# Kernel tuning notes

Measured on AMD Instinct MI355X. Metric: run time of the kernel, lower is better.

The kernel has to match this reference:

```python
import jax, jax.numpy as jnp
import numpy as np

N, C, T, V, S = 64, 64, 300, 25, 3
INTER = C // 4  # coff_embedding = 4
KER_T = 9      # temporal attention kernel
KER_V = V      # V=25 is odd -> spatial attention kernel = V, pad = (V-1)//2


def setup_inputs() -> dict:
    key = jax.random.key(0)
    ks = jax.random.split(key, 20)
    f = lambda k, s, scale=0.05: jax.random.normal(k, s, jnp.float32) * scale
    return {
        "x": jax.random.normal(ks[0], (N, C, T, V), jnp.float32),
        "A": f(ks[1], (S, V, V), 0.2),
        "alpha": jnp.array(0.1, jnp.float32),
        "Wa": f(ks[2], (S, INTER, C)), "ba": f(ks[3], (S, INTER)),
        "Wb": f(ks[4], (S, INTER, C)), "bb": f(ks[5], (S, INTER)),
        "Wd": f(ks[6], (S, C, C)),     "bd": f(ks[7], (S, C)),
        "bn_gamma": jnp.ones((C,), jnp.float32),
        "bn_beta": jnp.zeros((C,), jnp.float32),
        "bn_mean": f(ks[8], (C,)),
        "bn_var": jax.random.uniform(ks[9], (C,), jnp.float32) + 0.5,
        "Wsa": f(ks[10], (1, C, KER_V)), "bsa": f(ks[11], (1,)),
        "Wta": f(ks[12], (1, C, KER_T)), "bta": f(ks[13], (1,)),
        "Wfc1": f(ks[14], (C // 2, C)),  "bfc1": f(ks[15], (C // 2,)),
        "Wfc2": f(ks[16], (C, C // 2)),  "bfc2": f(ks[17], (C,)),
    }


def _conv1d(z, w, bias, pad):
    # z: [N, Cin, L], w: [Cout, Cin, K] -> [N, Cout, L]
    o = jax.lax.conv_general_dilated(z, w, (1,), [(pad, pad)],
                                     dimension_numbers=('NCH', 'OIH', 'NCH'))
    return o + bias[None, :, None]


def reference(x, A, alpha, Wa, ba, Wb, bb, Wd, bd,
              bn_gamma, bn_beta, bn_mean, bn_var,
              Wsa, bsa, Wta, bta, Wfc1, bfc1, Wfc2, bfc2):
    n, c, t, v = x.shape
    inter = Wa.shape[1]
    # adaptive adjacency per subset (1x1 convs = channel einsums)
    a = jnp.einsum('nctv,sic->nsitv', x, Wa) + ba[None, :, :, None, None]   # [N,S,inter,T,V]
    b = jnp.einsum('nctv,sic->nsitv', x, Wb) + bb[None, :, :, None, None]
    M = jnp.tanh(jnp.einsum('nsitv,nsitw->nsvw', a, b) / (inter * t))       # [N,S,V,V]
    G = A[None] + alpha * M
    # graph conv: x @ G per subset, then 1x1 conv_d, summed over subsets
    zp = jnp.einsum('nctv,nsvw->nsctw', x, G)                                # [N,S,C,T,V]
    y = jnp.einsum('nsctv,soc->notv', zp, Wd) + bd.sum(0)[None, :, None, None]
    # BN (eval) + residual (down = identity since in_c == out_c) + ReLU
    inv = bn_gamma / jnp.sqrt(bn_var + 1e-5)
    y = (y - bn_mean[None, :, None, None]) * inv[None, :, None, None] + bn_beta[None, :, None, None]
    y = jax.nn.relu(y + x)
    # spatial attention over joints
    se1 = jax.nn.sigmoid(_conv1d(y.mean(2), Wsa, bsa, (KER_V - 1) // 2))    # [N,1,V]
    y = y * se1[:, :, None, :] + y
    # temporal attention over frames
    se1 = jax.nn.sigmoid(_conv1d(y.mean(3), Wta, bta, (KER_T - 1) // 2))    # [N,1,T]
    y = y * se1[:, :, :, None] + y
    # channel attention (squeeze-excite)
    se = y.mean((2, 3))                                                      # [N,C]
    se2 = jax.nn.sigmoid(jax.nn.relu(se @ Wfc1.T + bfc1) @ Wfc2.T + bfc2)
    y = y * se2[:, :, None, None] + y
    return y
```

## Files before the change

kernel.cpp:

```cpp
#include <hip/hip_runtime.h>

typedef __bf16 bf16;
typedef bf16 bf16x8 __attribute__((ext_vector_type(8)));
typedef bf16 bf16x4 __attribute__((ext_vector_type(4)));
typedef float f32x4 __attribute__((ext_vector_type(4)));

#define WS_XG    0u
#define WS_WAB   61505536u
#define WS_WD    61517824u
#define WS_COEFA 61542400u
#define WS_COEFB 61542656u
#define WS_GT    61542912u
#define WS_MPART 61936128u
#define WS_STP   61936128u
#define WS_SVP   68489728u
#define WS_SE1   74519040u
#define WS_SE2   74527232u
#define WS_SE3   74605056u

__device__ __forceinline__ f32x4 mfma16(bf16x8 a, bf16x8 b, f32x4 c) {
  return __builtin_amdgcn_mfma_f32_16x16x32_bf16(a, b, c, 0, 0, 0);
}

__global__ __launch_bounds__(256) void k_prep(
    const float* __restrict__ Wa, const float* __restrict__ Wb,
    const float* __restrict__ Wd, const float* __restrict__ bd,
    const float* __restrict__ gam, const float* __restrict__ bet,
    const float* __restrict__ mean, const float* __restrict__ var,
    char* __restrict__ ws) {
  bf16* wab = (bf16*)(ws + WS_WAB);
  bf16* wd  = (bf16*)(ws + WS_WD);
  float* cA = (float*)(ws + WS_COEFA);
  float* cB = (float*)(ws + WS_COEFB);
  int tid = threadIdx.x;
  for (int f = tid; f < 3*32*64; f += 256) {
    int s = f >> 11, r = (f >> 6) & 31, c = f & 63;
    float v = (r < 16) ? Wa[(s*16 + r)*64 + c] : Wb[(s*16 + (r-16))*64 + c];
    wab[f] = (bf16)v;
  }
  for (int f = tid; f < 3*64*64; f += 256) wd[f] = (bf16)Wd[f];
  if (tid < 64) {
    float bds = bd[tid] + bd[64+tid] + bd[128+tid];
    float iv = gam[tid] / sqrtf(var[tid] + 1e-5f);
    cA[tid] = iv;
    cB[tid] = (bds - mean[tid]) * iv + bet[tid];
  }
}

__global__ __launch_bounds__(256) void k_tr(
    const float* __restrict__ x, char* __restrict__ ws) {
  __shared__ __attribute__((aligned(16))) bf16 tile[64*204];
  const int tc = blockIdx.x, n = blockIdx.y, tid = threadIdx.x;
  const int t0 = tc*8;
  const int vmax = min(200, 7500 - t0*25);
  bf16* XG = (bf16*)(ws + WS_XG);
  #pragma unroll
  for (int it = 0; it < 13; ++it) {
    int u = it*256 + tid;
    if (u < 3200) {
      int c = u / 50, q = u % 50;
      int idx = 4*q;
      if (idx < vmax) {
        float4 val = *(const float4*)(x + (size_t)(n*64 + c)*7500 + t0*25 + idx);
        bf16x4 pk = {(bf16)val.x, (bf16)val.y, (bf16)val.z, (bf16)val.w};
        *(bf16x4*)&tile[c*204 + idx] = pk;
      }
    }
  }
  __syncthreads();
  #pragma unroll
  for (int it = 0; it < 7; ++it) {
    int u = it*256 + tid;
    if (u < 1600) {
      int c8 = u & 7, tv = u >> 3;
      int t = t0 + tv/25, v = tv % 25;
      if (t < 300) {
        bf16x8 pk;
        #pragma unroll
        for (int j = 0; j < 8; ++j) pk[j] = tile[(c8*8 + j)*204 + tv];
        *(bf16x8*)&XG[((size_t)(n*300 + t)*25 + v)*64 + c8*8] = pk;
      }
    }
  }
}

__global__ __launch_bounds__(256) void k1_m(
    const float* __restrict__ ba_g, const float* __restrict__ bb_g,
    char* __restrict__ ws) {
  __shared__ __attribute__((aligned(16))) bf16 AB[6*32*72];
  const int seg = blockIdx.x, n = blockIdx.y;
  const int tid = threadIdx.x;
  const int lane = tid & 63, wv = tid >> 6;
  const int l15 = lane & 15, l4 = lane >> 4;
  const int t0 = seg*19, tlen = min(19, 300 - t0);
  const bf16* XG  = (const bf16*)(ws + WS_XG);
  const bf16* wab = (const bf16*)(ws + WS_WAB);
  const f32x4 z4 = {0.f,0.f,0.f,0.f};

  bf16x8 Afr[6][2];
  float bias[6][4];
  #pragma unroll
  for (int rt = 0; rt < 6; ++rt) {
    const int s = rt >> 1, abk = rt & 1;
    #pragma unroll
    for (int kk = 0; kk < 2; ++kk)
      Afr[rt][kk] = *(const bf16x8*)&wab[(s*32 + abk*16 + l15)*64 + kk*32 + 8*l4];
    const float* bp = abk ? bb_g : ba_g;
    #pragma unroll
    for (int r = 0; r < 4; ++r) bias[rt][r] = bp[s*16 + 4*l4 + r];
  }
  f32x4 macc[3]; macc[0]=z4; macc[1]=z4; macc[2]=z4;
  const int vt2 = wv >> 1, wt2 = wv & 1;
  const int nch = (tlen + 3) >> 2;

  for (int ch = 0; ch < nch; ++ch) {
    const int tl = ch*4 + wv;
    const int t = t0 + tl;
    const bool tv = (tl < tlen);
    #pragma unroll
    for (int vt = 0; vt < 2; ++vt) {
      f32x4 acc[6];
      #pragma unroll
      for (int rt = 0; rt < 6; ++rt) acc[rt] = z4;
      #pragma unroll
      for (int kk = 0; kk < 2; ++kk) {
        bf16x8 B = *(const bf16x8*)&XG[((size_t)(n*300 + t)*25 + vt*16 + l15)*64 + kk*32 + 8*l4];
        #pragma unroll
        for (int rt = 0; rt < 6; ++rt) acc[rt] = mfma16(Afr[rt][kk], B, acc[rt]);
      }
      #pragma unroll
      for (int rt = 0; rt < 6; ++rt) {
        bf16x4 pk;
        #pragma unroll
        for (int r = 0; r < 4; ++r)
          pk[r] = (bf16)(tv ? (acc[rt][r] + bias[rt][r]) : 0.f);
        *(bf16x4*)&AB[(rt*32 + vt*16 + l15)*72 + wv*16 + 4*l4] = pk;
      }
    }
    __syncthreads();
    #pragma unroll
    for (int s = 0; s < 3; ++s) {
      #pragma unroll
      for (int kk = 0; kk < 2; ++kk) {
        bf16x8 Aa = *(const bf16x8*)&AB[((s*2 + 0)*32 + vt2*16 + l15)*72 + kk*32 + 8*l4];
        bf16x8 Bb = *(const bf16x8*)&AB[((s*2 + 1)*32 + wt2*16 + l15)*72 + kk*32 + 8*l4];
        macc[s] = mfma16(Aa, Bb, macc[s]);
      }
    }
    __syncthreads();
  }
  float* mp = (float*)(ws + WS_MPART);
  #pragma unroll
  for (int s = 0; s < 3; ++s) {
    #pragma unroll
    for (int r = 0; r < 4; ++r) {
      int v = vt2*16 + 4*l4 + r, w = wt2*16 + l15;
      mp[(((n*16 + seg)*3 + s)*32 + v)*32 + w] = macc[s][r];
    }
  }
}

__global__ __launch_bounds__(256) void k1b_g(
    const float* __restrict__ A, const float* __restrict__ alp,
    char* __restrict__ ws) {
  int e = blockIdx.x*256 + threadIdx.x;
  int w = e & 31, v = (e >> 5) & 31;
  int s = (e >> 10) % 3, n = e / 3072;
  const float* mp = (const float*)(ws + WS_MPART);
  float m = 0.f;
  #pragma unroll
  for (int p = 0; p < 16; ++p)
    m += mp[(((n*16 + p)*3 + s)*32 + v)*32 + w];
  float g = 0.f;
  if (v < 25 && w < 25)
    g = A[(s*25 + v)*25 + w] + alp[0] * tanhf(m * (1.f/4800.f));
  bf16* gt = (bf16*)(ws + WS_GT);
  gt[((n*3 + s)*32 + w)*32 + v] = (bf16)g;
}

__global__ __launch_bounds__(256, 4) void k3_y(char* __restrict__ ws) {
  __shared__ __attribute__((aligned(16))) bf16 wdL[3*64*72];
  __shared__ __attribute__((aligned(16))) bf16 ULs[4*16*96];
  const int seg = blockIdx.x, n = blockIdx.y;
  const int tid = threadIdx.x, lane = tid & 63, wv = tid >> 6;
  const int l15 = lane & 15, l4 = lane >> 4;
  const int t0 = seg*19, tlen = min(19, 300 - t0);
  const bf16* XG = (const bf16*)(ws + WS_XG);
  bf16* YG = (bf16*)(ws + WS_XG);
  const bf16* wd = (const bf16*)(ws + WS_WD);
  const bf16* gt = (const bf16*)(ws + WS_GT);
  const float* cA = (const float*)(ws + WS_COEFA);
  const float* cB = (const float*)(ws + WS_COEFB);
  const f32x4 z4 = {0.f,0.f,0.f,0.f};
  bf16* UL = &ULs[wv*16*96];

  for (int f = tid; f < 1536; f += 256) {
    int row = f >> 3, c8 = f & 7;
    *(bf16x8*)&wdL[row*72 + c8*8] = *(const bf16x8*)&wd[row*64 + c8*8];
  }
  bf16x8 Gfr[2][3];
  #pragma unroll
  for (int wt = 0; wt < 2; ++wt)
    #pragma unroll
    for (int s = 0; s < 3; ++s)
      Gfr[wt][s] = *(const bf16x8*)&gt[((n*3 + s)*32 + wt*16 + l15)*32 + 8*l4];
  __syncthreads();

  const int tb = (tlen*wv) >> 2, te = (tlen*(wv+1)) >> 2;
  float st[4][2][4] = {};

  for (int tl = tb; tl < te; ++tl) {
    const size_t rowb = (size_t)(n*300 + t0 + tl)*25;
    bf16x8 Bv[2][2];
    #pragma unroll
    for (int vt = 0; vt < 2; ++vt)
      #pragma unroll
      for (int kk = 0; kk < 2; ++kk)
        Bv[vt][kk] = *(const bf16x8*)&XG[(rowb + vt*16 + l15)*64 + kk*32 + 8*l4];
    #pragma unroll
    for (int ot = 0; ot < 4; ++ot) {
      #pragma unroll
      for (int s = 0; s < 3; ++s) {
        bf16x8 W0 = *(const bf16x8*)&wdL[(s*64 + ot*16 + l15)*72 + 8*l4];
        bf16x8 W1 = *(const bf16x8*)&wdL[(s*64 + ot*16 + l15)*72 + 32 + 8*l4];
        #pragma unroll
        for (int vt = 0; vt < 2; ++vt) {
          f32x4 acc = mfma16(W0, Bv[vt][0], z4);
          acc = mfma16(W1, Bv[vt][1], acc);
          #pragma unroll
          for (int r = 0; r < 4; ++r)
            UL[(4*l4 + r)*96 + s*32 + vt*16 + l15] = (bf16)acc[r];
        }
      }
      f32x4 acc2[2] = {z4, z4};
      #pragma unroll
      for (int s = 0; s < 3; ++s) {
        bf16x8 Aa = *(const bf16x8*)&UL[l15*96 + s*32 + 8*l4];
        acc2[0] = mfma16(Aa, Gfr[0][s], acc2[0]);
        acc2[1] = mfma16(Aa, Gfr[1][s], acc2[1]);
      }
      const int o0 = ot*16 + 4*l4;
      const f32x4 cAr = *(const f32x4*)&cA[o0];
      const f32x4 cBr = *(const f32x4*)&cB[o0];
      #pragma unroll
      for (int wt = 0; wt < 2; ++wt) {
        const int w = wt*16 + l15;
        bf16x4 Rx = *(const bf16x4*)&XG[(rowb + w)*64 + o0];
        if (w < 25) {
          bf16x4 pk;
          #pragma unroll
          for (int r = 0; r < 4; ++r) {
            float val = fmaxf(acc2[wt][r]*cAr[r] + cBr[r] + (float)Rx[r], 0.f);
            pk[r] = (bf16)val;
            st[ot][wt][r] += val;
          }
          *(bf16x4*)&YG[(rowb + w)*64 + o0] = pk;
        }
      }
    }
  }
  float* LDSf = (float*)wdL;
  float* stp = (float*)(ws + WS_STP);
  #pragma unroll
  for (int half = 0; half < 2; ++half) {
    __syncthreads();
    #pragma unroll
    for (int ot2 = 0; ot2 < 2; ++ot2)
      #pragma unroll
      for (int wt = 0; wt < 2; ++wt)
        #pragma unroll
        for (int r = 0; r < 4; ++r)
          LDSf[wv*1056 + (ot2*16 + 4*l4 + r)*33 + wt*16 + l15] = st[half*2 + ot2][wt][r];
    __syncthreads();
    for (int e = tid; e < 800; e += 256) {
      int o = e / 25, w = e % 25;
      float sum = LDSf[o*33 + w] + LDSf[1056 + o*33 + w]
                + LDSf[2112 + o*33 + w] + LDSf[3168 + o*33 + w];
      stp[((n*16 + seg)*64 + half*32 + o)*25 + w] = sum;
    }
  }
}

__global__ __launch_bounds__(256) void k4_se1(
    const float* __restrict__ Wsa, const float* __restrict__ bsa,
    char* __restrict__ ws) {
  __shared__ float Sm[64][26];
  __shared__ float red[25][8];
  int n = blockIdx.x, tid = threadIdx.x;
  const float* stp = (const float*)(ws + WS_STP);
  for (int f = tid; f < 1600; f += 256) {
    int c = f / 25, v = f % 25;
    float s = 0.f;
    #pragma unroll
    for (int p = 0; p < 16; ++p) s += stp[((n*16 + p)*64 + c)*25 + v];
    Sm[c][v] = s * (1.f/300.f);
  }
  __syncthreads();
  float acc = 0.f;
  int v = tid >> 3, part = tid & 7;
  if (tid < 200) {
    for (int c = part; c < 64; c += 8) {
      #pragma unroll
      for (int k = 0; k < 25; ++k) {
        int vv = v + k - 12;
        if (vv >= 0 && vv < 25) acc += Wsa[c*25 + k] * Sm[c][vv];
      }
    }
    red[v][part] = acc;
  }
  __syncthreads();
  if (tid < 25) {
    float a = bsa[0];
    #pragma unroll
    for (int p = 0; p < 8; ++p) a += red[tid][p];
    ((float*)(ws + WS_SE1))[n*32 + tid] = 1.f + 1.f/(1.f + expf(-a));
  }
}

__global__ __launch_bounds__(256) void k5_sv(char* __restrict__ ws) {
  __shared__ float w1[25];
  const int tq = blockIdx.x, n = blockIdx.y;
  const int wv = threadIdx.x >> 6, lane = threadIdx.x & 63;
  const bf16* YG = (const bf16*)(ws + WS_XG);
  bf16* svp = (bf16*)(ws + WS_SVP);
  if (threadIdx.x < 25) w1[threadIdx.x] = ((const float*)(ws + WS_SE1))[n*32 + threadIdx.x];
  __syncthreads();
  const int tb = tq*75;
  for (int i = wv; i < 75; i += 4) {
    const int t = tb + i;
    float acc = 0.f;
    #pragma unroll
    for (int v = 0; v < 25; ++v)
      acc += w1[v] * (float)YG[(((size_t)n*300 + t)*25 + v)*64 + lane];
    svp[((size_t)n*304 + t)*64 + lane] = (bf16)acc;
  }
}

__global__ __launch_bounds__(1024) void k_att2(
    const float* __restrict__ Wta, const float* __restrict__ bta,
    const float* __restrict__ Wfc1, const float* __restrict__ bfc1,
    const float* __restrict__ Wfc2, const float* __restrict__ bfc2,
    char* __restrict__ ws) {
  __shared__ bf16 Sv[64][304];
  __shared__ float WLa[576];
  __shared__ float redt[304][4];
  __shared__ float w2s[304];
  __shared__ float red2[64][16];
  __shared__ float mS[64];
  __shared__ float hS[32];
  const int n = blockIdx.x, tid = threadIdx.x;
  const bf16* svp = (const bf16*)(ws + WS_SVP);

  for (int u = tid; u < 300*64; u += 1024) {
    int t = u >> 6, c = u & 63;
    Sv[c][t] = svp[((size_t)n*304 + t)*64 + c];
  }
  for (int f = tid; f < 576; f += 1024) WLa[f] = Wta[f];
  __syncthreads();
  for (int u = tid; u < 1200; u += 1024) {
    int t = u >> 2, part = u & 3;
    float acc = 0.f;
    for (int c = part*16; c < part*16 + 16; ++c) {
      #pragma unroll
      for (int k = 0; k < 9; ++k) {
        int t2 = t + k - 4;
        if (t2 >= 0 && t2 < 300) acc += WLa[c*9 + k] * (float)Sv[c][t2];
      }
    }
    redt[t][part] = acc;
  }
  __syncthreads();
  if (tid < 300) {
    float a = (redt[tid][0] + redt[tid][1] + redt[tid][2] + redt[tid][3]) * (1.f/25.f) + bta[0];
    float f2 = 1.f + 1.f/(1.f + expf(-a));
    w2s[tid] = f2;
    ((float*)(ws + WS_SE2))[n*304 + tid] = f2;
  }
  __syncthreads();
  {
    int c = tid & 63, part = tid >> 6;
    int tb = part*19, te = min(tb + 19, 300);
    float acc = 0.f;
    for (int t = tb; t < te; ++t) acc += w2s[t] * (float)Sv[c][t];
    red2[c][part] = acc;
  }
  __syncthreads();
  if (tid < 64) {
    float mm = 0.f;
    #pragma unroll
    for (int p = 0; p < 16; ++p) mm += red2[tid][p];
    mS[tid] = mm * (1.f/7500.f);
  }
  __syncthreads();
  if (tid < 32) {
    float a = bfc1[tid];
    for (int c = 0; c < 64; ++c) a += Wfc1[tid*64 + c] * mS[c];
    hS[tid] = fmaxf(a, 0.f);
  }
  __syncthreads();
  if (tid < 64) {
    float a = bfc2[tid];
    #pragma unroll
    for (int j = 0; j < 32; ++j) a += Wfc2[tid*32 + j] * hS[j];
    ((float*)(ws + WS_SE3))[n*64 + tid] = 1.f + 1.f/(1.f + expf(-a));
  }
}

__global__ __launch_bounds__(256) void k7_scale(
    const char* __restrict__ ws, float* __restrict__ out) {
  __shared__ float tile[200*65];
  __shared__ float w3S[64];
  const int tc = blockIdx.x, n = blockIdx.y, tid = threadIdx.x;
  const bf16* YG = (const bf16*)(ws + WS_XG);
  const float* w1 = (const float*)(ws + WS_SE1) + n*32;
  const float* w2 = (const float*)(ws + WS_SE2) + n*304;
  if (tid < 64) w3S[tid] = ((const float*)(ws + WS_SE3))[n*64 + tid];
  const int tb = tc*8;
  const int nT = min(8, 300 - tb);
  const int rowlen = nT*25;
  __syncthreads();
  for (int u = tid; u < rowlen*8; u += 256) {
    int c8 = u & 7, rest = u >> 3;
    int v = rest % 25, dt = rest / 25;
    int t = tb + dt;
    bf16x8 val = *(const bf16x8*)&YG[(((size_t)n*300 + t)*25 + v)*64 + c8*8];
    float sc = w1[v] * w2[t];
    #pragma unroll
    for (int j = 0; j < 8; ++j)
      tile[(dt*25 + v)*65 + c8*8 + j] = (float)val[j] * sc * w3S[c8*8 + j];
  }
  __syncthreads();
  const int nq2 = rowlen >> 1;
  for (int u = tid; u < 64*nq2; u += 256) {
    int c = u / nq2, q2 = u % nq2;
    float2 o;
    o.x = tile[(2*q2)*65 + c];
    o.y = tile[(2*q2 + 1)*65 + c];
    *(float2*)&out[(size_t)(n*64 + c)*7500 + tb*25 + 2*q2] = o;
  }
}

extern "C" void kernel_launch(void* const* d_in, const int* in_sizes, int n_in,
                              void* d_out, int out_size, void* d_ws, size_t ws_size,
                              hipStream_t stream) {
  const float* x    = (const float*)d_in[0];
  const float* A    = (const float*)d_in[1];
  const float* alp  = (const float*)d_in[2];
  const float* Wa   = (const float*)d_in[3];
  const float* ba   = (const float*)d_in[4];
  const float* Wb   = (const float*)d_in[5];
  const float* bb   = (const float*)d_in[6];
  const float* Wd   = (const float*)d_in[7];
  const float* bd   = (const float*)d_in[8];
  const float* gam  = (const float*)d_in[9];
  const float* bet  = (const float*)d_in[10];
  const float* mean = (const float*)d_in[11];
  const float* var  = (const float*)d_in[12];
  const float* Wsa  = (const float*)d_in[13];
  const float* bsa  = (const float*)d_in[14];
  const float* Wta  = (const float*)d_in[15];
  const float* bta  = (const float*)d_in[16];
  const float* Wfc1 = (const float*)d_in[17];
  const float* bfc1 = (const float*)d_in[18];
  const float* Wfc2 = (const float*)d_in[19];
  const float* bfc2 = (const float*)d_in[20];
  char* ws = (char*)d_ws;
  float* out = (float*)d_out;

  k_prep<<<dim3(1), dim3(256), 0, stream>>>(Wa, Wb, Wd, bd, gam, bet, mean, var, ws);
  k_tr<<<dim3(38, 64), dim3(256), 0, stream>>>(x, ws);
  k1_m<<<dim3(16, 64), dim3(256), 0, stream>>>(ba, bb, ws);
  k1b_g<<<dim3(768), dim3(256), 0, stream>>>(A, alp, ws);
  k3_y<<<dim3(16, 64), dim3(256), 0, stream>>>(ws);
  k4_se1<<<dim3(64), dim3(256), 0, stream>>>(Wsa, bsa, ws);
  k5_sv<<<dim3(4, 64), dim3(256), 0, stream>>>(ws);
  k_att2<<<dim3(64), dim3(1024), 0, stream>>>(Wta, bta, Wfc1, bfc1, Wfc2, bfc2, ws);
  k7_scale<<<dim3(38, 64), dim3(256), 0, stream>>>(ws, out);
}
```

Before: 248.4 us.

## Restructure adjacency kernel to per-wave register accumulation and vectorize scale kernels

k1_m now gives each wave its own time range and computes the a·b product directly from MFMA outputs in registers using a K=16 bf16 MFMA. This removes the per-chunk LDS staging and the two barriers per chunk, replacing them with one LDS reduction across waves at the end. k5_sv now loads 8 channels per thread with vector loads, and k7_scale uses smaller 4-frame tiles with twice as many blocks and unrolled loops. The cost is higher register pressure in k1_m, an occupancy hint of 3 blocks, and a final cross-wave reduction.

```diff
diff --git a/kernel.cpp b/kernel.cpp
--- a/kernel.cpp
+++ b/kernel.cpp
@@ -4,6 +4,7 @@
 typedef bf16 bf16x8 __attribute__((ext_vector_type(8)));
 typedef bf16 bf16x4 __attribute__((ext_vector_type(4)));
 typedef float f32x4 __attribute__((ext_vector_type(4)));
+typedef short s16x4 __attribute__((ext_vector_type(4)));
 
 #define WS_XG    0u
 #define WS_WAB   61505536u
@@ -21,6 +22,23 @@
 __device__ __forceinline__ f32x4 mfma16(bf16x8 a, bf16x8 b, f32x4 c) {
   return __builtin_amdgcn_mfma_f32_16x16x32_bf16(a, b, c, 0, 0, 0);
 }
+
+#if __has_builtin(__builtin_amdgcn_mfma_f32_16x16x16_bf16)
+__device__ __forceinline__ f32x4 mfma16k(bf16x4 a, bf16x4 b, f32x4 c) {
+  return __builtin_amdgcn_mfma_f32_16x16x16_bf16(a, b, c, 0, 0, 0);
+}
+#elif __has_builtin(__builtin_amdgcn_mfma_f32_16x16x16bf16_1k)
+__device__ __forceinline__ f32x4 mfma16k(bf16x4 a, bf16x4 b, f32x4 c) {
+  s16x4 ai = __builtin_bit_cast(s16x4, a);
+  s16x4 bi = __builtin_bit_cast(s16x4, b);
+  return __builtin_amdgcn_mfma_f32_16x16x16bf16_1k(ai, bi, c, 0, 0, 0);
+}
+#else
+__device__ __forceinline__ f32x4 mfma16k(bf16x4 a, bf16x4 b, f32x4 c) {
+  asm volatile("v_mfma_f32_16x16x16_bf16 %0, %1, %2, %0" : "+v"(c) : "v"(a), "v"(b));
+  return c;
+}
+#endif
 
 __global__ __launch_bounds__(256) void k_prep(
     const float* __restrict__ Wa, const float* __restrict__ Wb,
@@ -84,10 +102,10 @@
   }
 }
 
-__global__ __launch_bounds__(256) void k1_m(
+__global__ __launch_bounds__(256, 3) void k1_m(
     const float* __restrict__ ba_g, const float* __restrict__ bb_g,
     char* __restrict__ ws) {
-  __shared__ __attribute__((aligned(16))) bf16 AB[6*32*72];
+  __shared__ float red[4][32][33];
   const int seg = blockIdx.x, n = blockIdx.y;
   const int tid = threadIdx.x;
   const int lane = tid & 63, wv = tid >> 6;
@@ -109,53 +127,59 @@
     #pragma unroll
     for (int r = 0; r < 4; ++r) bias[rt][r] = bp[s*16 + 4*l4 + r];
   }
-  f32x4 macc[3]; macc[0]=z4; macc[1]=z4; macc[2]=z4;
-  const int vt2 = wv >> 1, wt2 = wv & 1;
-  const int nch = (tlen + 3) >> 2;
-
-  for (int ch = 0; ch < nch; ++ch) {
-    const int tl = ch*4 + wv;
-    const int t = t0 + tl;
-    const bool tv = (tl < tlen);
-    #pragma unroll
-    for (int vt = 0; vt < 2; ++vt) {
-      f32x4 acc[6];
-      #pragma unroll
-      for (int rt = 0; rt < 6; ++rt) acc[rt] = z4;
-      #pragma unroll
-      for (int kk = 0; kk < 2; ++kk) {
-        bf16x8 B = *(const bf16x8*)&XG[((size_t)(n*300 + t)*25 + vt*16 + l15)*64 + kk*32 + 8*l4];
-        #pragma unroll
-        for (int rt = 0; rt < 6; ++rt) acc[rt] = mfma16(Afr[rt][kk], B, acc[rt]);
-      }
-      #pragma unroll
-      for (int rt = 0; rt < 6; ++rt) {
-        bf16x4 pk;
+  f32x4 macc[3][2][2] = {};
+  const int tb = (tlen*wv) >> 2, te = (tlen*(wv+1)) >> 2;
+
+  for (int tl = tb; tl < te; ++tl) {
+    const size_t rowb = (size_t)(n*300 + t0 + tl)*25;
+    bf16x8 Bv[2][2];
+    #pragma unroll
+    for (int vt = 0; vt < 2; ++vt)
+      #pragma unroll
+      for (int kk = 0; kk < 2; ++kk)
+        Bv[vt][kk] = *(const bf16x8*)&XG[(rowb + vt*16 + l15)*64 + kk*32 + 8*l4];
+    #pragma unroll
+    for (int s = 0; s < 3; ++s) {
+      f32x4 acc[2][2];
+      #pragma unroll
+      for (int ab = 0; ab < 2; ++ab)
+        #pragma unroll
+        for (int vt = 0; vt < 2; ++vt) {
+          f32x4 a = mfma16(Afr[2*s + ab][0], Bv[vt][0], z4);
+          acc[ab][vt] = mfma16(Afr[2*s + ab][1], Bv[vt][1], a);
+        }
+      bf16x4 af[2], bf_[2];
+      #pragma unroll
+      for (int vt = 0; vt < 2; ++vt) {
+        #pragma unroll
+        for (int r = 0; r < 4; ++r) {
+          af[vt][r]  = (bf16)(acc[0][vt][r] + bias[2*s][r]);
+          bf_[vt][r] = (bf16)(acc[1][vt][r] + bias[2*s + 1][r]);
+        }
+      }
+      #pragma unroll
+      for (int vt = 0; vt < 2; ++vt)
+        #pragma unroll
+        for (int wt = 0; wt < 2; ++wt)
+          macc[s][vt][wt] = mfma16k(af[vt], bf_[wt], macc[s][vt][wt]);
+    }
+  }
+  float* mp = (float*)(ws + WS_MPART);
+  #pragma unroll
+  for (int s = 0; s < 3; ++s) {
+    __syncthreads();
+    #pragma unroll
+    for (int vt = 0; vt < 2; ++vt)
+      #pragma unroll
+      for (int wt = 0; wt < 2; ++wt)
         #pragma unroll
         for (int r = 0; r < 4; ++r)
-          pk[r] = (bf16)(tv ? (acc[rt][r] + bias[rt][r]) : 0.f);
-        *(bf16x4*)&AB[(rt*32 + vt*16 + l15)*72 + wv*16 + 4*l4] = pk;
-      }
-    }
+          red[wv][vt*16 + 4*l4 + r][wt*16 + l15] = macc[s][vt][wt][r];
     __syncthreads();
-    #pragma unroll
-    for (int s = 0; s < 3; ++s) {
-      #pragma unroll
-      for (int kk = 0; kk < 2; ++kk) {
-        bf16x8 Aa = *(const bf16x8*)&AB[((s*2 + 0)*32 + vt2*16 + l15)*72 + kk*32 + 8*l4];
-        bf16x8 Bb = *(const bf16x8*)&AB[((s*2 + 1)*32 + wt2*16 + l15)*72 + kk*32 + 8*l4];
-        macc[s] = mfma16(Aa, Bb, macc[s]);
-      }
-    }
-    __syncthreads();
-  }
-  float* mp = (float*)(ws + WS_MPART);
-  #pragma unroll
-  for (int s = 0; s < 3; ++s) {
-    #pragma unroll
-    for (int r = 0; r < 4; ++r) {
-      int v = vt2*16 + 4*l4 + r, w = wt2*16 + l15;
-      mp[(((n*16 + seg)*3 + s)*32 + v)*32 + w] = macc[s][r];
+    for (int e = tid; e < 1024; e += 256) {
+      int v = e >> 5, w = e & 31;
+      float sum = red[0][v][w] + red[1][v][w] + red[2][v][w] + red[3][v][w];
+      mp[(((n*16 + seg)*3 + s)*32 + v)*32 + w] = sum;
     }
   }
 }
@@ -320,19 +344,29 @@
 __global__ __launch_bounds__(256) void k5_sv(char* __restrict__ ws) {
   __shared__ float w1[25];
   const int tq = blockIdx.x, n = blockIdx.y;
-  const int wv = threadIdx.x >> 6, lane = threadIdx.x & 63;
+  const int tid = threadIdx.x;
   const bf16* YG = (const bf16*)(ws + WS_XG);
   bf16* svp = (bf16*)(ws + WS_SVP);
-  if (threadIdx.x < 25) w1[threadIdx.x] = ((const float*)(ws + WS_SE1))[n*32 + threadIdx.x];
-  __syncthreads();
-  const int tb = tq*75;
-  for (int i = wv; i < 75; i += 4) {
-    const int t = tb + i;
-    float acc = 0.f;
-    #pragma unroll
-    for (int v = 0; v < 25; ++v)
-      acc += w1[v] * (float)YG[(((size_t)n*300 + t)*25 + v)*64 + lane];
-    svp[((size_t)n*304 + t)*64 + lane] = (bf16)acc;
+  if (tid < 25) w1[tid] = ((const float*)(ws + WS_SE1))[n*32 + tid];
+  __syncthreads();
+  const int c8 = tid & 7, ts = tid >> 3;
+  #pragma unroll
+  for (int i = 0; i < 3; ++i) {
+    int tl = i*32 + ts;
+    if (tl < 75) {
+      const int t = tq*75 + tl;
+      float acc[8] = {};
+      #pragma unroll
+      for (int v = 0; v < 25; ++v) {
+        bf16x8 yv = *(const bf16x8*)&YG[(((size_t)n*300 + t)*25 + v)*64 + c8*8];
+        #pragma unroll
+        for (int j = 0; j < 8; ++j) acc[j] += w1[v] * (float)yv[j];
+      }
+      bf16x8 pk;
+      #pragma unroll
+      for (int j = 0; j < 8; ++j) pk[j] = (bf16)acc[j];
+      *(bf16x8*)&svp[((size_t)n*304 + t)*64 + c8*8] = pk;
+    }
   }
 }
 
@@ -408,35 +442,40 @@
 
 __global__ __launch_bounds__(256) void k7_scale(
     const char* __restrict__ ws, float* __restrict__ out) {
-  __shared__ float tile[200*65];
+  __shared__ float tile[100*65];
   __shared__ float w3S[64];
   const int tc = blockIdx.x, n = blockIdx.y, tid = threadIdx.x;
   const bf16* YG = (const bf16*)(ws + WS_XG);
   const float* w1 = (const float*)(ws + WS_SE1) + n*32;
   const float* w2 = (const float*)(ws + WS_SE2) + n*304;
   if (tid < 64) w3S[tid] = ((const float*)(ws + WS_SE3))[n*64 + tid];
-  const int tb = tc*8;
-  const int nT = min(8, 300 - tb);
-  const int rowlen = nT*25;
-  __syncthreads();
-  for (int u = tid; u < rowlen*8; u += 256) {
-    int c8 = u & 7, rest = u >> 3;
-    int v = rest % 25, dt = rest / 25;
-    int t = tb + dt;
-    bf16x8 val = *(const bf16x8*)&YG[(((size_t)n*300 + t)*25 + v)*64 + c8*8];
-    float sc = w1[v] * w2[t];
-    #pragma unroll
-    for (int j = 0; j < 8; ++j)
-      tile[(dt*25 + v)*65 + c8*8 + j] = (float)val[j] * sc * w3S[c8*8 + j];
-  }
-  __syncthreads();
-  const int nq2 = rowlen >> 1;
-  for (int u = tid; u < 64*nq2; u += 256) {
-    int c = u / nq2, q2 = u % nq2;
-    float2 o;
-    o.x = tile[(2*q2)*65 + c];
-    o.y = tile[(2*q2 + 1)*65 + c];
-    *(float2*)&out[(size_t)(n*64 + c)*7500 + tb*25 + 2*q2] = o;
+  const int tb = tc*4;
+  __syncthreads();
+  #pragma unroll
+  for (int it = 0; it < 4; ++it) {
+    int u = it*256 + tid;
+    if (u < 800) {
+      int c8 = u & 7, rest = u >> 3;
+      int v = rest % 25, dt = rest / 25;
+      int t = tb + dt;
+      bf16x8 val = *(const bf16x8*)&YG[(((size_t)n*300 + t)*25 + v)*64 + c8*8];
+      float sc = w1[v] * w2[t];
+      #pragma unroll
+      for (int j = 0; j < 8; ++j)
+        tile[(dt*25 + v)*65 + c8*8 + j] = (float)val[j] * sc * w3S[c8*8 + j];
+    }
+  }
+  __syncthreads();
+  #pragma unroll
+  for (int it = 0; it < 13; ++it) {
+    int u = it*256 + tid;
+    if (u < 3200) {
+      int c = u / 50, q2 = u % 50;
+      float2 o;
+      o.x = tile[(2*q2)*65 + c];
+      o.y = tile[(2*q2 + 1)*65 + c];
+      *(float2*)&out[(size_t)(n*64 + c)*7500 + tb*25 + 2*q2] = o;
+    }
   }
 }
 
@@ -475,5 +514,5 @@
   k4_se1<<<dim3(64), dim3(256), 0, stream>>>(Wsa, bsa, ws);
   k5_sv<<<dim3(4, 64), dim3(256), 0, stream>>>(ws);
   k_att2<<<dim3(64), dim3(1024), 0, stream>>>(Wta, bta, Wfc1, bfc1, Wfc2, bfc2, ws);
-  k7_scale<<<dim3(38, 64), dim3(256), 0, stream>>>(ws, out);
-}
+  k7_scale<<<dim3(75, 64), dim3(256), 0, stream>>>(ws, out);
+}
```

Result: faster. 236.6 us (-4.8%).
